# Optimization experiments

Measured on AMD Instinct MI355X. Metric: run time of the kernel, lower is better.

Reference implementation:

```python
import jax, jax.numpy as jnp
import numpy as np

B, N_PER, E_PER = 32, 2048, 4096          # graphs, nodes/graph, edges/graph
NN, NE = B * N_PER, B * E_PER              # 65536 nodes, 131072 edges
F_IN, EMB, H, OUT, VOCAB = 32, 32, 128, 64, 10000


def _glorot(k, shape):
    lim = float(np.sqrt(6.0 / (shape[0] + shape[-1])))
    return jax.random.uniform(k, shape, jnp.float32, -lim, lim)


def setup_inputs() -> dict:
    key = jax.random.key(0)
    ks = jax.random.split(key, 20)
    x = jax.random.normal(ks[0], (NN, F_IN), jnp.float32)
    node_index = jax.random.randint(ks[1], (NN,), 0, VOCAB)
    # intra-graph edges, nodes sorted by graph -> edge batch is sorted too
    off = jnp.repeat(jnp.arange(B) * N_PER, E_PER)
    src = jax.random.randint(ks[2], (NE,), 0, N_PER) + off
    dst = jax.random.randint(ks[3], (NE,), 0, N_PER) + off
    edge_index = jnp.stack([src, dst])
    d_in = F_IN + EMB
    return dict(
        x=x, node_index=node_index, edge_index=edge_index,
        emb=jax.random.normal(ks[4], (VOCAB, EMB), jnp.float32),
        W1=_glorot(ks[5], (d_in, H)), a1s=_glorot(ks[6], (H,)), a1d=_glorot(ks[7], (H,)), b1=jnp.zeros((H,), jnp.float32),
        W2=_glorot(ks[8], (H, H)),   a2s=_glorot(ks[9], (H,)), a2d=_glorot(ks[10], (H,)), b2=jnp.zeros((H,), jnp.float32),
        W3=_glorot(ks[11], (H, H)),  a3s=_glorot(ks[12], (H,)), a3d=_glorot(ks[13], (H,)), b3=jnp.zeros((H,), jnp.float32),
        fcW=_glorot(ks[14], (2 * H, H)), fcb=jnp.zeros((H,), jnp.float32),
        Wz=_glorot(ks[15], (H + OUT, OUT)), bz=jnp.zeros((OUT,), jnp.float32),
        Wr=_glorot(ks[16], (H + OUT, OUT)), br=jnp.zeros((OUT,), jnp.float32),
        Wh=_glorot(ks[17], (H + OUT, OUT)), bh=jnp.zeros((OUT,), jnp.float32),
    )


def _gat(h_in, W, a_s, a_d, b, src, dst):
    # single-head GATConv with self-loops already appended to (src, dst)
    h = h_in @ W                                              # [NN, H]
    e = jax.nn.leaky_relu((h @ a_s)[src] + (h @ a_d)[dst], 0.2)  # [E']
    m = jax.ops.segment_max(e, dst, num_segments=NN)
    ex = jnp.exp(e - m[dst])
    s = jax.ops.segment_sum(ex, dst, num_segments=NN)
    alpha = ex / s[dst]
    return jax.ops.segment_sum(h[src] * alpha[:, None], dst, num_segments=NN) + b


def reference(x, node_index, edge_index, emb, W1, a1s, a1d, b1, W2, a2s, a2d, b2,
              W3, a3s, a3d, b3, fcW, fcb, Wz, bz, Wr, br, Wh, bh):
    gelu = lambda v: jax.nn.gelu(v, approximate=False)  # torch F.gelu default = erf
    h = jnp.concatenate([x, emb[node_index]], axis=1)   # [NN, F_IN+EMB]
    loops = jnp.arange(NN)
    src = jnp.concatenate([edge_index[0], loops])
    dst = jnp.concatenate([edge_index[1], loops])
    h = gelu(_gat(h, W1, a1s, a1d, b1, src, dst))
    h = gelu(_gat(h, W2, a2s, a2d, b2, src, dst))
    h = gelu(_gat(h, W3, a3s, a3d, b3, src, dst))
    # per-edge features (original edges, no self-loops)
    ef = jnp.concatenate([h[edge_index[0]], h[edge_index[1]]], axis=-1)  # [NE, 2H]
    ef = gelu(ef @ fcW + fcb)                                            # [NE, H]
    # equal-size graphs, edges sorted by graph -> construct_tensor == reshape, mask all-ones
    gru_in = ef.reshape(B, E_PER, H).transpose(1, 0, 2)                  # [T, B, H]

    def step(hid, xt):
        c = jnp.concatenate([xt, hid], axis=1)
        z = jax.nn.sigmoid(c @ Wz + bz)
        r = jax.nn.sigmoid(c @ Wr + br)
        cr = jnp.concatenate([xt, r * hid], axis=1)
        ht = jax.nn.leaky_relu(cr @ Wh + bh, 0.01)
        return (1 - z) * hid + z * ht, None

    hid, _ = jax.lax.scan(step, jnp.zeros((B, OUT), ef.dtype), gru_in)
    # predict_graph=True with all-ones mask -> prediction at last timestep == final hidden
    return hid
```

## Files before the change

kernel.cpp:

```cpp
#include <hip/hip_runtime.h>
#include <hip/hip_bf16.h>
#include <math.h>

#define NN_ 65536
#define NE_ 131072
#define B_  32
#define T_  4096
#define D_  8

typedef __fp16 f16x2 __attribute__((ext_vector_type(2)));
typedef unsigned int u32;

__device__ __forceinline__ float gelu_f(float x){
    return 0.5f*x*(1.0f + erff(x*0.70710678118654752f));
}

__device__ __forceinline__ unsigned enc_f(float f){
    unsigned b = __float_as_uint(f);
    return (b & 0x80000000u) ? ~b : (b | 0x80000000u);
}
__device__ __forceinline__ float dec_f(unsigned u){
    return (u & 0x80000000u) ? __uint_as_float(u ^ 0x80000000u) : __uint_as_float(~u);
}

__device__ __forceinline__ int rdlane_i(int v, int l){
    return __builtin_amdgcn_readlane(v, l);
}
__device__ __forceinline__ int h2i(f16x2 h){ union{int i; f16x2 h;} u; u.h=h; return u.i; }
__device__ __forceinline__ f16x2 i2h(int i){ union{int i; f16x2 h;} u; u.i=i; return u.h; }

__device__ __forceinline__ float dot2(f16x2 a, f16x2 b, float c){
#if __has_builtin(__builtin_amdgcn_fdot2)
    return __builtin_amdgcn_fdot2(a, b, c, false);
#else
    return c + (float)a.x*(float)b.x + (float)a.y*(float)b.y;
#endif
}

__device__ __forceinline__ void gload_lds4(const float* g, float* l, int lane){
#if __has_builtin(__builtin_amdgcn_global_load_lds)
    __builtin_amdgcn_global_load_lds((const __attribute__((address_space(1))) u32*)g,
                                     (__attribute__((address_space(3))) u32*)l, 4, 0, 0);
#else
    l[lane] = *g;
#endif
}

__global__ void k_zero(float* p, int n){
    int i = blockIdx.x*blockDim.x + threadIdx.x;
    int stride = gridDim.x*blockDim.x;
    for(; i<n; i+=stride) p[i] = 0.f;
}

__global__ void k_embed(const float* __restrict__ x, const int* __restrict__ nidx,
                        const float* __restrict__ emb, float* __restrict__ h64){
    int gid = blockIdx.x*256 + threadIdx.x;
    int n = gid >> 6, c = gid & 63;
    float v = (c < 32) ? x[(size_t)n*32 + c] : emb[(size_t)nidx[n]*32 + (c-32)];
    h64[gid] = v;
}

template<int K>
__global__ void k_gemm_node(const float* __restrict__ A, const float* __restrict__ W,
                            float* __restrict__ C){
    int lane = threadIdx.x & 63;
    int wy = threadIdx.x >> 6;
    int r0 = blockIdx.x*16 + wy*4;
    const float* a0 = A + (size_t)r0*K;
    float acc0[4] = {0,0,0,0}, acc1[4] = {0,0,0,0};
    #pragma unroll 4
    for(int k=0;k<K;k+=4){
        float4 av[4];
        #pragma unroll
        for(int i=0;i<4;i++) av[i] = *(const float4*)(a0 + (size_t)i*K + k);
        #pragma unroll
        for(int kk=0;kk<4;kk++){
            float w0 = W[(size_t)(k+kk)*128 + lane];
            float w1 = W[(size_t)(k+kk)*128 + 64 + lane];
            #pragma unroll
            for(int i=0;i<4;i++){
                float a = ((const float*)&av[i])[kk];
                acc0[i] += a*w0;
                acc1[i] += a*w1;
            }
        }
    }
    #pragma unroll
    for(int i=0;i<4;i++){
        C[(size_t)(r0+i)*128 + lane]      = acc0[i];
        C[(size_t)(r0+i)*128 + 64 + lane] = acc1[i];
    }
}

__global__ void k_rowdots(const float* __restrict__ hW, const float* __restrict__ as_,
                          const float* __restrict__ ad_, float* __restrict__ ssrc,
                          float* __restrict__ sdst){
    int lane = threadIdx.x & 63;
    int row = blockIdx.x*4 + (threadIdx.x >> 6);
    const float* hp = hW + (size_t)row*128;
    float h0 = hp[lane], h1 = hp[lane+64];
    float d0 = h0*as_[lane] + h1*as_[lane+64];
    float d1 = h0*ad_[lane] + h1*ad_[lane+64];
    #pragma unroll
    for(int off=32; off; off>>=1){
        d0 += __shfl_xor(d0, off);
        d1 += __shfl_xor(d1, off);
    }
    if(lane==0){ ssrc[row] = d0; sdst[row] = d1; }
}

__global__ void k_edge1(const int* __restrict__ src, const int* __restrict__ dst,
                        const float* __restrict__ ssrc, const float* __restrict__ sdst,
                        float* __restrict__ ebuf, unsigned* __restrict__ menc){
    int e = blockIdx.x*256 + threadIdx.x;
    int s, d;
    if(e < NE_){ s = src[e]; d = dst[e]; } else { s = d = e - NE_; }
    float v = ssrc[s] + sdst[d];
    v = (v > 0.f) ? v : 0.2f*v;
    ebuf[e] = v;
    atomicMax(&menc[d], enc_f(v));
}

__global__ void k_edge2(const int* __restrict__ dst, const unsigned* __restrict__ menc,
                        float* __restrict__ ebuf, float* __restrict__ ssum){
    int e = blockIdx.x*256 + threadIdx.x;
    int d = (e < NE_) ? dst[e] : (e - NE_);
    float m = dec_f(menc[d]);
    float ex = __expf(ebuf[e] - m);
    ebuf[e] = ex;
    atomicAdd(&ssum[d], ex);
}

__global__ void __launch_bounds__(256) k_edge3_lds(
        const int* __restrict__ src, const int* __restrict__ dst,
        const float* __restrict__ ebuf, const float* __restrict__ ssum,
        const float* __restrict__ hW, const float* __restrict__ bias,
        float* __restrict__ hAgg){
    __shared__ float agg[2048][8];
    int g  = blockIdx.x;
    int c0 = blockIdx.y << 3;
    int t  = threadIdx.x;
    int cc = t & 7;
    int elane = t >> 3;

    for(int idx = t; idx < 2048*8; idx += 256)
        ((float*)agg)[idx] = 0.f;
    __syncthreads();

    const int gbase_e = g << 12;
    const int gbase_n = g << 11;
    for(int i = 0; i < 192; i++){
        int eg = i*32 + elane;
        int s, dloc; float a;
        if(eg < 4096){
            int e = gbase_e + eg;
            s    = src[e];
            int d = dst[e];
            dloc = d - gbase_n;
            a    = ebuf[e] / ssum[d];
        } else {
            int nl = eg - 4096;
            s    = gbase_n + nl;
            dloc = nl;
            a    = ebuf[NE_ + gbase_n + nl] / ssum[gbase_n + nl];
        }
        float v = hW[(size_t)s*128 + c0 + cc] * a;
        atomicAdd(&agg[dloc][cc], v);
    }
    __syncthreads();

    for(int idx = t; idx < 2048*8; idx += 256){
        int nl = idx >> 3;
        int ch = c0 + (idx & 7);
        hAgg[((size_t)(gbase_n + nl))*128 + ch] = gelu_f(agg[nl][idx & 7] + bias[ch]);
    }
}

__global__ void k_ef_x3(const float* __restrict__ h3, const int* __restrict__ src,
                        const int* __restrict__ dst, const float* __restrict__ fcW,
                        const float* __restrict__ fcb,
                        const float* __restrict__ Wz, const float* __restrict__ Wr,
                        const float* __restrict__ Wh, const float* __restrict__ bz,
                        const float* __restrict__ br, const float* __restrict__ bh,
                        float* __restrict__ X3){
    __shared__ float efs[16][128];
    int lane = threadIdx.x & 63;
    int wy = threadIdx.x >> 6;
    int e0 = blockIdx.x*16 + wy*4;

    {
        float acc0[4] = {0,0,0,0}, acc1[4] = {0,0,0,0};
        #pragma unroll
        for(int half=0; half<2; half++){
            const float* rowp[4];
            #pragma unroll
            for(int i=0;i<4;i++){
                int n = (half==0) ? src[e0+i] : dst[e0+i];
                rowp[i] = h3 + (size_t)n*128;
            }
            #pragma unroll 2
            for(int k=0;k<128;k+=4){
                float4 av[4];
                #pragma unroll
                for(int i=0;i<4;i++) av[i] = *(const float4*)(rowp[i] + k);
                #pragma unroll
                for(int kk=0;kk<4;kk++){
                    int kw = half*128 + k + kk;
                    float w0 = fcW[(size_t)kw*128 + lane];
                    float w1 = fcW[(size_t)kw*128 + 64 + lane];
                    #pragma unroll
                    for(int i=0;i<4;i++){
                        float a = ((const float*)&av[i])[kk];
                        acc0[i] += a*w0;
                        acc1[i] += a*w1;
                    }
                }
            }
        }
        float b0 = fcb[lane], b1 = fcb[64+lane];
        #pragma unroll
        for(int i=0;i<4;i++){
            efs[wy*4+i][lane]      = gelu_f(acc0[i] + b0);
            efs[wy*4+i][64 + lane] = gelu_f(acc1[i] + b1);
        }
    }
    __syncthreads();
    {
        float accz[4] = {0,0,0,0}, accr[4] = {0,0,0,0}, acch[4] = {0,0,0,0};
        #pragma unroll 2
        for(int k=0;k<128;k+=4){
            #pragma unroll
            for(int kk=0;kk<4;kk++){
                float w0 = Wz[(size_t)(k+kk)*64 + lane];
                float w1 = Wr[(size_t)(k+kk)*64 + lane];
                float w2 = Wh[(size_t)(k+kk)*64 + lane];
                #pragma unroll
                for(int i=0;i<4;i++){
                    float a = efs[wy*4+i][k+kk];
                    accz[i] += a*w0;
                    accr[i] += a*w1;
                    acch[i] += a*w2;
                }
            }
        }
        float b0 = bz[lane], b1 = br[lane], b2 = bh[lane];
        #pragma unroll
        for(int i=0;i<4;i++){
            int e = e0 + i;
            int bb = e >> 12;
            int t  = e & 4095;
            float* o = X3 + ((size_t)t*32 + bb)*192;
            o[lane]       = accz[i] + b0;
            o[64 + lane]  = accr[i] + b1;
            o[128 + lane] = acch[i] + b2;
        }
    }
}

__global__ void __launch_bounds__(256) k_gru(const float* __restrict__ X3,
                       const float* __restrict__ Wz, const float* __restrict__ Wr,
                       const float* __restrict__ Wh, float* __restrict__ out){
    __shared__ float  ring[D_][192];
    __shared__ float2 P1[4][64];
    __shared__ float  P2[4][64];
    int b = blockIdx.x;
    int j = threadIdx.x & 63;
    int w = __builtin_amdgcn_readfirstlane(threadIdx.x >> 6);
    int kbase = w << 4;
    int odd = j & 1;

    f16x2 wzp[8], wrp[8], whp[8];
    #pragma unroll
    for(int i=0;i<8;i++){
        int r0 = 128 + kbase + 2*i;
        wzp[i] = __builtin_amdgcn_cvt_pkrtz(Wz[(size_t)r0*64 + j], Wz[(size_t)(r0+1)*64 + j]);
        wrp[i] = __builtin_amdgcn_cvt_pkrtz(Wr[(size_t)r0*64 + j], Wr[(size_t)(r0+1)*64 + j]);
        whp[i] = __builtin_amdgcn_cvt_pkrtz(Wh[(size_t)r0*64 + j], Wh[(size_t)(r0+1)*64 + j]);
    }

    if(w == 0){
        for(int s=0;s<D_;s++){
            const float* gp = X3 + ((size_t)s*32 + b)*192 + j;
            gload_lds4(gp,       &ring[s][0],   j);
            gload_lds4(gp + 64,  &ring[s][64],  j);
            gload_lds4(gp + 128, &ring[s][128], j);
        }
        asm volatile("s_waitcnt vmcnt(21)" ::: "memory");
        __builtin_amdgcn_sched_barrier(0);
    }
    __builtin_amdgcn_s_barrier();

    float h = 0.f;
    for(int step=0; step<T_; step++){
        int sl = step & (D_-1);
        float xz = ring[sl][j], xr = ring[sl][64+j], xh = ring[sl][128+j];

        float hn = __shfl_xor(h, 1);
        int hp = h2i(__builtin_amdgcn_cvt_pkrtz(odd ? hn : h, odd ? h : hn));

        float az0=0.f, az1=0.f, ar0=0.f, ar1=0.f;
        #pragma unroll
        for(int i=0;i<8;i+=2){
            f16x2 h0 = i2h(rdlane_i(hp, kbase + 2*i));
            f16x2 h1 = i2h(rdlane_i(hp, kbase + 2*i + 2));
            az0 = dot2(h0, wzp[i],   az0); ar0 = dot2(h0, wrp[i],   ar0);
            az1 = dot2(h1, wzp[i+1], az1); ar1 = dot2(h1, wrp[i+1], ar1);
        }
        P1[w][j] = make_float2(az0+az1, ar0+ar1);
        asm volatile("s_waitcnt lgkmcnt(0)" ::: "memory");
        __builtin_amdgcn_s_barrier();

        if(w == 0){
            int ps = (step + D_ < T_) ? (step + D_) : (T_-1);
            const float* gp = X3 + ((size_t)ps*32 + b)*192 + j;
            gload_lds4(gp,       &ring[sl][0],   j);
            gload_lds4(gp + 64,  &ring[sl][64],  j);
            gload_lds4(gp + 128, &ring[sl][128], j);
        }

        float2 q0 = P1[0][j], q1 = P1[1][j], q2 = P1[2][j], q3 = P1[3][j];
        float sz = xz + ((q0.x+q1.x)+(q2.x+q3.x));
        float sr = xr + ((q0.y+q1.y)+(q2.y+q3.y));
        float z = __builtin_amdgcn_rcpf(1.f + __expf(-sz));
        float r = __builtin_amdgcn_rcpf(1.f + __expf(-sr));
        float rh = r*h;

        float rn = __shfl_xor(rh, 1);
        int rp = h2i(__builtin_amdgcn_cvt_pkrtz(odd ? rn : rh, odd ? rh : rn));

        float ah0=0.f, ah1=0.f;
        #pragma unroll
        for(int i=0;i<8;i+=2){
            f16x2 r0 = i2h(rdlane_i(rp, kbase + 2*i));
            f16x2 r1 = i2h(rdlane_i(rp, kbase + 2*i + 2));
            ah0 = dot2(r0, whp[i],   ah0);
            ah1 = dot2(r1, whp[i+1], ah1);
        }
        P2[w][j] = ah0 + ah1;
        if(w == 0){
            asm volatile("s_waitcnt vmcnt(21)" ::: "memory");
        }
        asm volatile("s_waitcnt lgkmcnt(0)" ::: "memory");
        __builtin_amdgcn_s_barrier();

        float s2 = xh + ((P2[0][j]+P2[1][j]) + (P2[2][j]+P2[3][j]));
        float ht = fmaxf(s2, 0.01f*s2);
        h = fmaf(z, ht - h, h);
    }
    if(w == 0) out[(size_t)b*64 + j] = h;
}

extern "C" void kernel_launch(void* const* d_in, const int* in_sizes, int n_in,
                              void* d_out, int out_size, void* d_ws, size_t ws_size,
                              hipStream_t stream) {
    const float* x    = (const float*)d_in[0];
    const int*   nidx = (const int*)d_in[1];
    const int*   src  = (const int*)d_in[2];
    const int*   dst  = src + NE_;
    const float* emb  = (const float*)d_in[3];
    const float* W1 = (const float*)d_in[4];
    const float* a1s = (const float*)d_in[5];
    const float* a1d = (const float*)d_in[6];
    const float* b1 = (const float*)d_in[7];
    const float* W2 = (const float*)d_in[8];
    const float* a2s = (const float*)d_in[9];
    const float* a2d = (const float*)d_in[10];
    const float* b2 = (const float*)d_in[11];
    const float* W3 = (const float*)d_in[12];
    const float* a3s = (const float*)d_in[13];
    const float* a3d = (const float*)d_in[14];
    const float* b3 = (const float*)d_in[15];
    const float* fcW = (const float*)d_in[16];
    const float* fcb = (const float*)d_in[17];
    const float* Wz = (const float*)d_in[18];
    const float* bz = (const float*)d_in[19];
    const float* Wr = (const float*)d_in[20];
    const float* br = (const float*)d_in[21];
    const float* Wh = (const float*)d_in[22];
    const float* bh = (const float*)d_in[23];
    float* out = (float*)d_out;

    float* ws = (float*)d_ws;
    float* hAgg = ws;
    float* X3   = hAgg + (size_t)NN_*128;
    float* bufA = X3;
    float* h64  = bufA + (size_t)NN_*128;
    float* ssrc = h64  + (size_t)NN_*64;
    float* sdst = ssrc + NN_;
    float* ssum = sdst + NN_;
    unsigned* menc = (unsigned*)(ssum + NN_);
    float* ebuf = (float*)menc + NN_;

    const int EP = NE_ + NN_;

    k_embed<<<NN_*64/256, 256, 0, stream>>>(x, nidx, emb, h64);

    const float* Ws[3]  = {W1, W2, W3};
    const float* as_[3] = {a1s, a2s, a3s};
    const float* ad_[3] = {a1d, a2d, a3d};
    const float* bs[3]  = {b1, b2, b3};

    for(int l=0; l<3; l++){
        if(l == 0)
            k_gemm_node<64><<<NN_/16, 256, 0, stream>>>(h64, Ws[l], bufA);
        else
            k_gemm_node<128><<<NN_/16, 256, 0, stream>>>(hAgg, Ws[l], bufA);
        k_zero<<<512, 256, 0, stream>>>(ssum, 2*NN_);
        k_rowdots<<<NN_/4, 256, 0, stream>>>(bufA, as_[l], ad_[l], ssrc, sdst);
        k_edge1<<<EP/256, 256, 0, stream>>>(src, dst, ssrc, sdst, ebuf, menc);
        k_edge2<<<EP/256, 256, 0, stream>>>(dst, menc, ebuf, ssum);
        k_edge3_lds<<<dim3(B_, 16), 256, 0, stream>>>(src, dst, ebuf, ssum, bufA, bs[l], hAgg);
    }

    k_ef_x3<<<NE_/16, 256, 0, stream>>>(hAgg, src, dst, fcW, fcb,
                                        Wz, Wr, Wh, bz, br, bh, X3);
    k_gru<<<B_, 256, 0, stream>>>(X3, Wz, Wr, Wh, out);
}
```

Before: 3.846 ms.

## Fold zeroing into rowdots, widen edge aggregation channels, simplify GRU h packing

Three independent changes. The separate zeroing kernel is removed and its work (ssum and menc reset) moves into k_rowdots, saving one launch per layer. The LDS edge aggregation now handles 16 channels per block instead of 8, with the edge loop unrolled by 4 so loads are batched; this halves the redundant src/dst/alpha reads but doubles LDS use to 128 KB and halves the grid to 256 blocks. In the serial GRU, the xor-shuffle-and-pack of h is replaced by direct readlanes plus cvt_pkrtz, which removes a cross-lane shuffle from the critical path but doubles the readlane count.

```diff
diff --git a/kernel.cpp b/kernel.cpp
--- a/kernel.cpp
+++ b/kernel.cpp
@@ -23,11 +23,9 @@
     return (u & 0x80000000u) ? __uint_as_float(u ^ 0x80000000u) : __uint_as_float(~u);
 }
 
-__device__ __forceinline__ int rdlane_i(int v, int l){
-    return __builtin_amdgcn_readlane(v, l);
-}
-__device__ __forceinline__ int h2i(f16x2 h){ union{int i; f16x2 h;} u; u.h=h; return u.i; }
-__device__ __forceinline__ f16x2 i2h(int i){ union{int i; f16x2 h;} u; u.i=i; return u.h; }
+__device__ __forceinline__ float rdlane(float v, int l){
+    return __int_as_float(__builtin_amdgcn_readlane(__float_as_int(v), l));
+}
 
 __device__ __forceinline__ float dot2(f16x2 a, f16x2 b, float c){
 #if __has_builtin(__builtin_amdgcn_fdot2)
@@ -44,12 +42,6 @@
 #else
     l[lane] = *g;
 #endif
-}
-
-__global__ void k_zero(float* p, int n){
-    int i = blockIdx.x*blockDim.x + threadIdx.x;
-    int stride = gridDim.x*blockDim.x;
-    for(; i<n; i+=stride) p[i] = 0.f;
 }
 
 __global__ void k_embed(const float* __restrict__ x, const int* __restrict__ nidx,
@@ -94,7 +86,8 @@
 
 __global__ void k_rowdots(const float* __restrict__ hW, const float* __restrict__ as_,
                           const float* __restrict__ ad_, float* __restrict__ ssrc,
-                          float* __restrict__ sdst){
+                          float* __restrict__ sdst, float* __restrict__ ssum,
+                          unsigned* __restrict__ menc){
     int lane = threadIdx.x & 63;
     int row = blockIdx.x*4 + (threadIdx.x >> 6);
     const float* hp = hW + (size_t)row*128;
@@ -106,7 +99,10 @@
         d0 += __shfl_xor(d0, off);
         d1 += __shfl_xor(d1, off);
     }
-    if(lane==0){ ssrc[row] = d0; sdst[row] = d1; }
+    if(lane==0){
+        ssrc[row] = d0; sdst[row] = d1;
+        ssum[row] = 0.f; menc[row] = 0u;
+    }
 }
 
 __global__ void k_edge1(const int* __restrict__ src, const int* __restrict__ dst,
@@ -136,43 +132,50 @@
         const float* __restrict__ ebuf, const float* __restrict__ ssum,
         const float* __restrict__ hW, const float* __restrict__ bias,
         float* __restrict__ hAgg){
-    __shared__ float agg[2048][8];
+    __shared__ float agg[2048][16];
     int g  = blockIdx.x;
-    int c0 = blockIdx.y << 3;
+    int c0 = blockIdx.y << 4;
     int t  = threadIdx.x;
-    int cc = t & 7;
-    int elane = t >> 3;
-
-    for(int idx = t; idx < 2048*8; idx += 256)
+    int cc = t & 15;
+    int elane = t >> 4;
+
+    for(int idx = t; idx < 2048*16; idx += 256)
         ((float*)agg)[idx] = 0.f;
     __syncthreads();
 
     const int gbase_e = g << 12;
     const int gbase_n = g << 11;
-    for(int i = 0; i < 192; i++){
-        int eg = i*32 + elane;
-        int s, dloc; float a;
-        if(eg < 4096){
-            int e = gbase_e + eg;
-            s    = src[e];
-            int d = dst[e];
-            dloc = d - gbase_n;
-            a    = ebuf[e] / ssum[d];
-        } else {
-            int nl = eg - 4096;
-            s    = gbase_n + nl;
-            dloc = nl;
-            a    = ebuf[NE_ + gbase_n + nl] / ssum[gbase_n + nl];
-        }
-        float v = hW[(size_t)s*128 + c0 + cc] * a;
-        atomicAdd(&agg[dloc][cc], v);
+    for(int i0 = 0; i0 < 384; i0 += 4){
+        int   s_[4], dl_[4];
+        float a_[4];
+        #pragma unroll
+        for(int u=0;u<4;u++){
+            int eg = (i0+u)*16 + elane;
+            if(eg < 4096){
+                int e = gbase_e + eg;
+                s_[u]  = src[e];
+                int d  = dst[e];
+                dl_[u] = d - gbase_n;
+                a_[u]  = ebuf[e] / ssum[d];
+            } else {
+                int nl = eg - 4096;
+                s_[u]  = gbase_n + nl;
+                dl_[u] = nl;
+                a_[u]  = ebuf[NE_ + gbase_n + nl] / ssum[gbase_n + nl];
+            }
+        }
+        #pragma unroll
+        for(int u=0;u<4;u++){
+            float v = hW[(size_t)s_[u]*128 + c0 + cc] * a_[u];
+            atomicAdd(&agg[dl_[u]][cc], v);
+        }
     }
     __syncthreads();
 
-    for(int idx = t; idx < 2048*8; idx += 256){
-        int nl = idx >> 3;
-        int ch = c0 + (idx & 7);
-        hAgg[((size_t)(gbase_n + nl))*128 + ch] = gelu_f(agg[nl][idx & 7] + bias[ch]);
+    for(int idx = t; idx < 2048*16; idx += 256){
+        int nl = idx >> 4;
+        int ch = c0 + (idx & 15);
+        hAgg[((size_t)(gbase_n + nl))*128 + ch] = gelu_f(agg[nl][idx & 15] + bias[ch]);
     }
 }
 
@@ -267,7 +270,6 @@
     int j = threadIdx.x & 63;
     int w = __builtin_amdgcn_readfirstlane(threadIdx.x >> 6);
     int kbase = w << 4;
-    int odd = j & 1;
 
     f16x2 wzp[8], wrp[8], whp[8];
     #pragma unroll
@@ -295,14 +297,13 @@
         int sl = step & (D_-1);
         float xz = ring[sl][j], xr = ring[sl][64+j], xh = ring[sl][128+j];
 
-        float hn = __shfl_xor(h, 1);
-        int hp = h2i(__builtin_amdgcn_cvt_pkrtz(odd ? hn : h, odd ? h : hn));
-
         float az0=0.f, az1=0.f, ar0=0.f, ar1=0.f;
         #pragma unroll
         for(int i=0;i<8;i+=2){
-            f16x2 h0 = i2h(rdlane_i(hp, kbase + 2*i));
-            f16x2 h1 = i2h(rdlane_i(hp, kbase + 2*i + 2));
+            f16x2 h0 = __builtin_amdgcn_cvt_pkrtz(rdlane(h, kbase+2*i),
+                                                  rdlane(h, kbase+2*i+1));
+            f16x2 h1 = __builtin_amdgcn_cvt_pkrtz(rdlane(h, kbase+2*i+2),
+                                                  rdlane(h, kbase+2*i+3));
             az0 = dot2(h0, wzp[i],   az0); ar0 = dot2(h0, wrp[i],   ar0);
             az1 = dot2(h1, wzp[i+1], az1); ar1 = dot2(h1, wrp[i+1], ar1);
         }
@@ -325,14 +326,13 @@
         float r = __builtin_amdgcn_rcpf(1.f + __expf(-sr));
         float rh = r*h;
 
-        float rn = __shfl_xor(rh, 1);
-        int rp = h2i(__builtin_amdgcn_cvt_pkrtz(odd ? rn : rh, odd ? rh : rn));
-
         float ah0=0.f, ah1=0.f;
         #pragma unroll
         for(int i=0;i<8;i+=2){
-            f16x2 r0 = i2h(rdlane_i(rp, kbase + 2*i));
-            f16x2 r1 = i2h(rdlane_i(rp, kbase + 2*i + 2));
+            f16x2 r0 = __builtin_amdgcn_cvt_pkrtz(rdlane(rh, kbase+2*i),
+                                                  rdlane(rh, kbase+2*i+1));
+            f16x2 r1 = __builtin_amdgcn_cvt_pkrtz(rdlane(rh, kbase+2*i+2),
+                                                  rdlane(rh, kbase+2*i+3));
             ah0 = dot2(r0, whp[i],   ah0);
             ah1 = dot2(r1, whp[i+1], ah1);
         }
@@ -405,11 +405,10 @@
             k_gemm_node<64><<<NN_/16, 256, 0, stream>>>(h64, Ws[l], bufA);
         else
             k_gemm_node<128><<<NN_/16, 256, 0, stream>>>(hAgg, Ws[l], bufA);
-        k_zero<<<512, 256, 0, stream>>>(ssum, 2*NN_);
-        k_rowdots<<<NN_/4, 256, 0, stream>>>(bufA, as_[l], ad_[l], ssrc, sdst);
+        k_rowdots<<<NN_/4, 256, 0, stream>>>(bufA, as_[l], ad_[l], ssrc, sdst, ssum, menc);
         k_edge1<<<EP/256, 256, 0, stream>>>(src, dst, ssrc, sdst, ebuf, menc);
         k_edge2<<<EP/256, 256, 0, stream>>>(dst, menc, ebuf, ssum);
-        k_edge3_lds<<<dim3(B_, 16), 256, 0, stream>>>(src, dst, ebuf, ssum, bufA, bs[l], hAgg);
+        k_edge3_lds<<<dim3(B_, 8), 256, 0, stream>>>(src, dst, ebuf, ssum, bufA, bs[l], hAgg);
     }
 
     k_ef_x3<<<NE_/16, 256, 0, stream>>>(hAgg, src, dst, fcW, fcb,
```

Result: slower. 3.928 ms (+2.1%).
